# Performance work log

Hardware: AMD Instinct MI355X
Metric: run time of the kernel (lower is better)

## Reference

```python
import jax, jax.numpy as jnp
import numpy as np

EMBED_DIM = 1024
NUM_HEADS = 16
HEAD_DIM = EMBED_DIM // NUM_HEADS
SCALE = HEAD_DIM ** -0.5


def setup_inputs() -> dict:
    key = jax.random.key(0)
    ks = jax.random.split(key, 7)
    B, S, D = 4, 2048, EMBED_DIM
    return {
        "x": jax.random.normal(ks[0], (B, S, D), dtype=jnp.float32),
        "gamma": jnp.ones((D,), dtype=jnp.float32),
        "beta": jnp.zeros((D,), dtype=jnp.float32),
        "w_qkv": jax.random.normal(ks[1], (D, 3 * D), dtype=jnp.float32) * (D ** -0.5),
        "b_qkv": jax.random.normal(ks[2], (3 * D,), dtype=jnp.float32) * 0.02,
        "w_proj": jax.random.normal(ks[3], (D, D), dtype=jnp.float32) * (D ** -0.5),
        "b_proj": jax.random.normal(ks[4], (D,), dtype=jnp.float32) * 0.02,
    }


def reference(x, gamma, beta, w_qkv, b_qkv, w_proj, b_proj):
    B, S, D = x.shape
    # pre-norm LayerNorm (eps=1e-5, torch default)
    mu = jnp.mean(x, axis=-1, keepdims=True)
    var = jnp.mean(jnp.square(x - mu), axis=-1, keepdims=True)
    xn = (x - mu) * jax.lax.rsqrt(var + 1e-5) * gamma + beta
    # fused QKV projection -> (3, B, H, S, hd)
    qkv = (xn @ w_qkv + b_qkv).reshape(B, S, 3, NUM_HEADS, HEAD_DIM)
    qkv = jnp.transpose(qkv, (2, 0, 3, 1, 4))
    q, k, v = qkv[0], qkv[1], qkv[2]
    scores = jnp.einsum("bhqd,bhkd->bhqk", q, k) * SCALE
    attn = jax.nn.softmax(scores, axis=-1)  # dropout p=0 -> no-op
    ctx = jnp.einsum("bhqk,bhkd->bhqd", attn, v)
    ctx = jnp.transpose(ctx, (0, 2, 1, 3)).reshape(B, S, D)
    return ctx @ w_proj + b_proj
```

## Files before the change

### kernel.cpp

```cpp
#include <hip/hip_runtime.h>

typedef unsigned short ushort_t;
typedef __attribute__((ext_vector_type(8))) short bf16x8;
typedef __attribute__((ext_vector_type(4))) float f32x4;
typedef __attribute__((ext_vector_type(16))) float f32x16;
typedef __attribute__((ext_vector_type(2))) __bf16 bf16v2;

#define BN 4
#define SEQ 2048
#define DIM 1024
#define NH 16
#define HDIM 64
#define MROWS (BN*SEQ)
#define QSCALE 0.18033688011112042f

__device__ __forceinline__ float bf2f(ushort_t s){ return __uint_as_float(((unsigned)s) << 16); }
__device__ __forceinline__ ushort_t f2bf(float f){
  unsigned u = __float_as_uint(f);
  u += 0x7fffu + ((u >> 16) & 1u);
  return (ushort_t)(u >> 16);
}
__device__ __forceinline__ unsigned pack2(float a, float b){
  return (unsigned)f2bf(a) | ((unsigned)f2bf(b) << 16);
}

#define GLL16(gp, lp) __builtin_amdgcn_global_load_lds( \
    (const __attribute__((address_space(1))) void*)(gp), \
    (__attribute__((address_space(3))) void*)(lp), 16, 0, 0)

__global__ __launch_bounds__(256) void ln_kernel(const float* __restrict__ x,
                                                 const float* __restrict__ gamma,
                                                 const float* __restrict__ beta,
                                                 ushort_t* __restrict__ xnb)
{
  int row = blockIdx.x;
  int t = threadIdx.x;
  float4 v = ((const float4*)(x + (size_t)row * DIM))[t];
  float s = v.x+v.y+v.z+v.w;
  float ss = v.x*v.x+v.y*v.y+v.z*v.z+v.w*v.w;
  #pragma unroll
  for (int o = 32; o > 0; o >>= 1){ s += __shfl_down(s, o); ss += __shfl_down(ss, o); }
  __shared__ float red[10];
  int wid = t >> 6;
  if ((t & 63) == 0){ red[wid] = s; red[4+wid] = ss; }
  __syncthreads();
  if (t == 0){
    float S0 = red[0]+red[1]+red[2]+red[3];
    float SS = red[4]+red[5]+red[6]+red[7];
    float mu = S0 * (1.f/DIM);
    float var = SS * (1.f/DIM) - mu*mu;
    red[8] = mu; red[9] = rsqrtf(var + 1e-5f);
  }
  __syncthreads();
  float mu = red[8], rstd = red[9];
  float4 g = ((const float4*)gamma)[t];
  float4 b = ((const float4*)beta)[t];
  float f0 = (v.x - mu)*rstd*g.x + b.x;
  float f1 = (v.y - mu)*rstd*g.y + b.y;
  float f2 = (v.z - mu)*rstd*g.z + b.z;
  float f3 = (v.w - mu)*rstd*g.w + b.w;
  *(uint2*)(xnb + (size_t)row*DIM + t*4) = make_uint2(pack2(f0,f1), pack2(f2,f3));
}

__global__ __launch_bounds__(256) void cvt_t(const float* __restrict__ src,
                                             ushort_t* __restrict__ dst,
                                             int K, int N, float qscale)
{
  __shared__ float tile[64][65];
  int k0 = blockIdx.y*64, n0 = blockIdx.x*64;
  float sc = (n0 < 1024) ? qscale : 1.f;
  int t = threadIdx.x;
  int c = (t & 15) * 4, r = t >> 4;
  #pragma unroll
  for (int p = 0; p < 4; p++){
    float4 v = *(const float4*)(src + (size_t)(k0 + r + p*16)*N + n0 + c);
    tile[r+p*16][c]   = v.x; tile[r+p*16][c+1] = v.y;
    tile[r+p*16][c+2] = v.z; tile[r+p*16][c+3] = v.w;
  }
  __syncthreads();
  #pragma unroll
  for (int p = 0; p < 4; p++){
    int nn = r + p*16;
    ushort4 o;
    o.x = f2bf(tile[c+0][nn]*sc); o.y = f2bf(tile[c+1][nn]*sc);
    o.z = f2bf(tile[c+2][nn]*sc); o.w = f2bf(tile[c+3][nn]*sc);
    *(ushort4*)(dst + (size_t)(n0+nn)*K + k0 + c) = o;
  }
}

__global__ __launch_bounds__(256) void vtrans(const ushort_t* __restrict__ V,
                                              ushort_t* __restrict__ vt)
{
  __shared__ ushort_t tile[64][72];
  int bh = blockIdx.x >> 5, sc = blockIdx.x & 31;
  int t = threadIdx.x;
  const ushort_t* src = V + ((size_t)bh*SEQ + sc*64)*HDIM;
  #pragma unroll
  for (int p = 0; p < 2; p++){
    int idx = p*256 + t;
    int r = idx >> 3, c8 = (idx & 7)*8;
    *(uint4*)&tile[r][c8] = *(const uint4*)(src + (size_t)r*HDIM + c8);
  }
  __syncthreads();
  ushort_t* dstp = vt + ((size_t)(bh*32 + sc))*HDIM*64;
  #pragma unroll
  for (int p = 0; p < 2; p++){
    int idx = p*256 + t;
    int d = idx >> 3, c8 = (idx & 7)*8;
    uint4 u;
    u.x = (unsigned)tile[c8+0][d] | ((unsigned)tile[c8+1][d] << 16);
    u.y = (unsigned)tile[c8+2][d] | ((unsigned)tile[c8+3][d] << 16);
    u.z = (unsigned)tile[c8+4][d] | ((unsigned)tile[c8+5][d] << 16);
    u.w = (unsigned)tile[c8+6][d] | ((unsigned)tile[c8+7][d] << 16);
    *(uint4*)(dstp + (size_t)d*64 + c8) = u;
  }
}

template<int MODE, int NCOLS>
__global__ __launch_bounds__(256) void mfma_gemm(
    const ushort_t* __restrict__ A,
    const ushort_t* __restrict__ BT,
    const float* __restrict__ bias,
    void* __restrict__ Cv)
{
  __shared__ __align__(16) unsigned char smem[17408];
  ushort_t* AsL = (ushort_t*)smem;
  ushort_t* BsL = (ushort_t*)(smem + 8192);

  int t = threadIdx.x;
  int lane = t & 63, w = t >> 6;
  int col = lane & 15, quad = lane >> 4;
  int n0 = blockIdx.x * 128, m0 = blockIdx.y * 128;

  f32x4 acc[4][4];
  #pragma unroll
  for (int i = 0; i < 4; i++)
    #pragma unroll
    for (int j = 0; j < 4; j++) acc[i][j] = (f32x4){0.f,0.f,0.f,0.f};

  int mbase = (w & 1)*64 + col;
  int nbase = (w >> 1)*64 + col;

  int r0 = (2*w  )*16 + (lane >> 2);
  int r1 = (2*w+1)*16 + (lane >> 2);
  int c0 = (((lane & 3) ^ ((r0 & 3) ^ ((r0 >> 2) & 3))) << 3);
  int c1 = (((lane & 3) ^ ((r1 & 3) ^ ((r1 >> 2) & 3))) << 3);
  const ushort_t* gA0 = A  + (size_t)(m0 + r0)*DIM + c0;
  const ushort_t* gA1 = A  + (size_t)(m0 + r1)*DIM + c1;
  const ushort_t* gB0 = BT + (size_t)(n0 + r0)*DIM + c0;
  const ushort_t* gB1 = BT + (size_t)(n0 + r1)*DIM + c1;
  unsigned char* lA0 = smem        + (2*w  )*1024;
  unsigned char* lA1 = smem        + (2*w+1)*1024;
  unsigned char* lB0 = smem + 8192 + (2*w  )*1024;
  unsigned char* lB1 = smem + 8192 + (2*w+1)*1024;

  int ppos = ((quad ^ ((col & 3) ^ ((col >> 2) & 3))) << 3);

  for (int k0 = 0; k0 < DIM; k0 += 32){
    __syncthreads();
    GLL16(gA0 + k0, lA0);
    GLL16(gA1 + k0, lA1);
    GLL16(gB0 + k0, lB0);
    GLL16(gB1 + k0, lB1);
    __syncthreads();

    bf16x8 af[4], bfr[4];
    #pragma unroll
    for (int i = 0; i < 4; i++){
      af[i]  = *(const bf16x8*)&AsL[(mbase + i*16)*32 + ppos];
      bfr[i] = *(const bf16x8*)&BsL[(nbase + i*16)*32 + ppos];
    }
    #pragma unroll
    for (int mt = 0; mt < 4; mt++)
      #pragma unroll
      for (int nt = 0; nt < 4; nt++)
        acc[mt][nt] = __builtin_amdgcn_mfma_f32_16x16x32_bf16(af[mt], bfr[nt], acc[mt][nt], 0, 0, 0);
  }

  float bscale = (MODE == 2 && n0 < 1024) ? QSCALE : 1.f;
  float bv[4];
  #pragma unroll
  for (int nt = 0; nt < 4; nt++) bv[nt] = bias[n0 + (w>>1)*64 + nt*16 + col] * bscale;

  if (MODE == 2){
    ushort_t (*Cs)[136] = (ushort_t(*)[136])smem;
    ushort_t* C = (ushort_t*)Cv;
    #pragma unroll
    for (int ph = 0; ph < 2; ph++){
      __syncthreads();
      if ((w & 1) == ph){
        #pragma unroll
        for (int mt = 0; mt < 4; mt++)
          #pragma unroll
          for (int nt = 0; nt < 4; nt++)
            #pragma unroll
            for (int r = 0; r < 4; r++)
              Cs[mt*16 + quad*4 + r][(w>>1)*64 + nt*16 + col] = f2bf(acc[mt][nt][r] + bv[nt]);
      }
      __syncthreads();
      #pragma unroll
      for (int p = 0; p < 4; p++){
        int id = p*256 + t;
        int row = id >> 4, cc = id & 15;
        uint4 u = *(const uint4*)&Cs[row][cc*8];
        int m = m0 + ph*64 + row;
        int n = n0 + cc*8;
        int which = n >> 10, hh = (n >> 6) & 15, d = n & 63;
        int b_ = m >> 11, s_ = m & (SEQ-1);
        *(uint4*)&C[((((size_t)which*BN + b_)*NH + hh)*SEQ + s_)*HDIM + d] = u;
      }
    }
  } else {
    float (*Cf)[132] = (float(*)[132])smem;
    float* C = (float*)Cv;
    #pragma unroll
    for (int ph = 0; ph < 4; ph++){
      __syncthreads();
      if ((w & 1) == (ph >> 1)){
        #pragma unroll
        for (int mi = 0; mi < 2; mi++){
          int mt = (ph & 1)*2 + mi;
          #pragma unroll
          for (int nt = 0; nt < 4; nt++)
            #pragma unroll
            for (int r = 0; r < 4; r++)
              Cf[mi*16 + quad*4 + r][(w>>1)*64 + nt*16 + col] = acc[mt][nt][r] + bv[nt];
        }
      }
      __syncthreads();
      #pragma unroll
      for (int p = 0; p < 4; p++){
        int id = p*256 + t;
        int row = id >> 5, cc = id & 31;
        float4 v = *(const float4*)&Cf[row][cc*4];
        int m = m0 + ph*32 + row;
        *(float4*)(C + (size_t)m*NCOLS + n0 + cc*4) = v;
      }
    }
  }
}

__global__ __launch_bounds__(512) void attn_kernel(const ushort_t* __restrict__ qkv,
                                                   const ushort_t* __restrict__ vtp,
                                                   ushort_t* __restrict__ ctx)
{
  __shared__ __align__(16) unsigned char lds[53248];
  ushort_t* Ksm = (ushort_t*)lds;
  ushort_t* Vsm = (ushort_t*)(lds + 8192);

  int t = threadIdx.x;
  int lane = t & 63, w = t >> 6;
  int m32 = lane & 31, half = lane >> 5;
  int r7 = m32 & 7;
  int id = blockIdx.x;
  int bh = (id & 7) | ((id >> 6) << 3);
  int qb = (id >> 3) & 7;

  const size_t PL = (size_t)BN * NH * SEQ * HDIM;
  const ushort_t* Qg = qkv + (size_t)bh * (SEQ * HDIM);
  const ushort_t* Kg = Qg + PL;
  const ushort_t* Vt = vtp + (size_t)bh * 32 * (HDIM * 64);
  int qbase = qb*256 + w*32;

  bf16x8 qf[4];
  #pragma unroll
  for (int c = 0; c < 4; c++)
    qf[c] = *(const bf16x8*)(Qg + (size_t)(qbase + m32)*HDIM + c*16 + half*8);

  bf16x8 ones;
  #pragma unroll
  for (int i = 0; i < 8; i++) ones[i] = (short)0x3F80;

  f32x16 accO[2], accL;
  #pragma unroll
  for (int i = 0; i < 2; i++)
    #pragma unroll
    for (int r = 0; r < 16; r++) accO[i][r] = 0.f;
  #pragma unroll
  for (int r = 0; r < 16; r++) accL[r] = 0.f;

  int srow = t >> 3, och = t & 7;
  const ushort_t* kp0 = Kg + (size_t)srow*HDIM + och*8;
  const ushort_t* vp0 = Vt + (size_t)srow*64 + och*8;
  int wofs = srow*64 + ((och ^ (srow & 7)) << 3);

  uint4 kr = *(const uint4*)kp0;
  uint4 vr = *(const uint4*)vp0;

  for (int kt = 0; kt < 32; kt++){
    __syncthreads();
    *(uint4*)&Ksm[wofs] = kr;
    *(uint4*)&Vsm[wofs] = vr;
    __syncthreads();

    if (kt < 31){
      kr = *(const uint4*)(kp0 + (size_t)(kt+1)*64*HDIM);
      vr = *(const uint4*)(vp0 + (size_t)(kt+1)*HDIM*64);
    }

    bf16x8 pb[4];
    #pragma unroll
    for (int mt = 0; mt < 2; mt++){
      f32x16 z;
      #pragma unroll
      for (int r = 0; r < 16; r++) z[r] = 0.f;
      int rowb = (mt*32 + m32) * 64;
      #pragma unroll
      for (int c = 0; c < 4; c++){
        bf16x8 af = *(const bf16x8*)&Ksm[rowb + (((2*c + half) ^ r7) << 3)];
        z = __builtin_amdgcn_mfma_f32_32x32x16_bf16(af, qf[c], z, 0, 0, 0);
      }
      unsigned u[8];
      #pragma unroll
      for (int i = 0; i < 8; i++){
        float p0 = __builtin_amdgcn_exp2f(z[2*i]);
        float p1 = __builtin_amdgcn_exp2f(z[2*i+1]);
        bf16v2 hh; hh.x = (__bf16)p0; hh.y = (__bf16)p1;
        u[i] = __builtin_bit_cast(unsigned, hh);
      }
      #pragma unroll
      for (int cc = 0; cc < 2; cc++){
        union { uint4 q; bf16x8 b; } cvt;
        cvt.q = make_uint4(u[4*cc+0], u[4*cc+1], u[4*cc+2], u[4*cc+3]);
        pb[mt*2 + cc] = cvt.b;
      }
    }

    #pragma unroll
    for (int kc = 0; kc < 4; kc++){
      accL = __builtin_amdgcn_mfma_f32_32x32x16_bf16(ones, pb[kc], accL, 0, 0, 0);
      #pragma unroll
      for (int md = 0; md < 2; md++){
        int dd = md*32 + m32;
        int rowb = dd * 64;
        union { bf16x8 v8; uint2 u2[2]; } vv;
        vv.u2[0] = *(const uint2*)&Vsm[rowb + (((2*kc  ) ^ r7) << 3) + 4*half];
        vv.u2[1] = *(const uint2*)&Vsm[rowb + (((2*kc+1) ^ r7) << 3) + 4*half];
        accO[md] = __builtin_amdgcn_mfma_f32_32x32x16_bf16(vv.v8, pb[kc], accO[md], 0, 0, 0);
      }
    }
  }

  float inv = 1.f / accL[0];

  ushort_t (*Os)[72] = (ushort_t(*)[72])(lds + 16384 + w*4608);
  #pragma unroll
  for (int md = 0; md < 2; md++)
    #pragma unroll
    for (int g = 0; g < 4; g++){
      int d0 = 8*g + 4*half + 32*md;
      unsigned lo = pack2(accO[md][4*g+0]*inv, accO[md][4*g+1]*inv);
      unsigned hi = pack2(accO[md][4*g+2]*inv, accO[md][4*g+3]*inv);
      *(uint2*)&Os[m32][d0] = make_uint2(lo, hi);
    }

  int b_ = bh >> 4, h_ = bh & 15;
  #pragma unroll
  for (int k = 0; k < 4; k++){
    int row = k*8 + (lane >> 3);
    uint4 u = *(const uint4*)&Os[row][(lane & 7)*8];
    *(uint4*)(ctx + ((size_t)(b_*SEQ + qb*256 + w*32 + row))*DIM + h_*HDIM + (lane & 7)*8) = u;
  }
}

extern "C" void kernel_launch(void* const* d_in, const int* in_sizes, int n_in,
                              void* d_out, int out_size, void* d_ws, size_t ws_size,
                              hipStream_t stream)
{
  const float* x      = (const float*)d_in[0];
  const float* gamma  = (const float*)d_in[1];
  const float* beta   = (const float*)d_in[2];
  const float* w_qkv  = (const float*)d_in[3];
  const float* b_qkv  = (const float*)d_in[4];
  const float* w_proj = (const float*)d_in[5];
  const float* b_proj = (const float*)d_in[6];

  char* ws = (char*)d_ws;
  ushort_t* wqkvT  = (ushort_t*)ws;
  ushort_t* vt     = (ushort_t*)ws;
  ushort_t* wprojT = (ushort_t*)ws;
  ushort_t* qkv    = (ushort_t*)(ws + 16u*1024*1024);
  ushort_t* Vplane = (ushort_t*)(ws + 48u*1024*1024);
  ushort_t* ctx    = (ushort_t*)(ws + 48u*1024*1024);
  ushort_t* xnb    = (ushort_t*)d_out;

  ln_kernel<<<MROWS, 256, 0, stream>>>(x, gamma, beta, xnb);
  cvt_t<<<dim3(3*DIM/64, DIM/64), 256, 0, stream>>>(w_qkv, wqkvT, DIM, 3*DIM, QSCALE);
  mfma_gemm<2, 3*DIM><<<dim3(3*DIM/128, MROWS/128), 256, 0, stream>>>(
      xnb, wqkvT, b_qkv, qkv);
  vtrans<<<BN*NH*(SEQ/64), 256, 0, stream>>>(Vplane, vt);
  attn_kernel<<<BN*NH*(SEQ/256), 512, 0, stream>>>(qkv, vt, ctx);
  cvt_t<<<dim3(DIM/64, DIM/64), 256, 0, stream>>>(w_proj, wprojT, DIM, DIM, 1.f);
  mfma_gemm<0, DIM><<<dim3(DIM/128, MROWS/128), 256, 0, stream>>>(
      ctx, wprojT, b_proj, d_out);
}
```

Measured before the change: 305.1 us.

## Software-pipeline attention loop so QK^T of next tile overlaps PV of current

```diff
diff --git a/kernel.cpp b/kernel.cpp
--- a/kernel.cpp
+++ b/kernel.cpp
@@ -284,37 +284,36 @@
   const ushort_t* vp0 = Vt + (size_t)srow*64 + och*8;
   int wofs = srow*64 + ((och ^ (srow & 7)) << 3);
 
+  int rowb0 = (m32) * 64;
+  int rowb1 = (32 + m32) * 64;
+
   uint4 kr = *(const uint4*)kp0;
   uint4 vr = *(const uint4*)vp0;
-
-  for (int kt = 0; kt < 32; kt++){
-    __syncthreads();
-    *(uint4*)&Ksm[wofs] = kr;
+  *(uint4*)&Ksm[wofs] = kr;
+  kr = *(const uint4*)(kp0 + (size_t)64*HDIM);
+  __syncthreads();
+
+  bf16x8 pb[4];
+  {
+    f32x16 z0, z1;
+    #pragma unroll
+    for (int r = 0; r < 16; r++){ z0[r] = 0.f; z1[r] = 0.f; }
+    #pragma unroll
+    for (int c = 0; c < 4; c++){
+      bf16x8 a0 = *(const bf16x8*)&Ksm[rowb0 + (((2*c + half) ^ r7) << 3)];
+      bf16x8 a1 = *(const bf16x8*)&Ksm[rowb1 + (((2*c + half) ^ r7) << 3)];
+      z0 = __builtin_amdgcn_mfma_f32_32x32x16_bf16(a0, qf[c], z0, 0, 0, 0);
+      z1 = __builtin_amdgcn_mfma_f32_32x32x16_bf16(a1, qf[c], z1, 0, 0, 0);
+    }
     *(uint4*)&Vsm[wofs] = vr;
-    __syncthreads();
-
-    if (kt < 31){
-      kr = *(const uint4*)(kp0 + (size_t)(kt+1)*64*HDIM);
-      vr = *(const uint4*)(vp0 + (size_t)(kt+1)*HDIM*64);
-    }
-
-    bf16x8 pb[4];
+    vr = *(const uint4*)(vp0 + (size_t)HDIM*64);
     #pragma unroll
     for (int mt = 0; mt < 2; mt++){
-      f32x16 z;
-      #pragma unroll
-      for (int r = 0; r < 16; r++) z[r] = 0.f;
-      int rowb = (mt*32 + m32) * 64;
-      #pragma unroll
-      for (int c = 0; c < 4; c++){
-        bf16x8 af = *(const bf16x8*)&Ksm[rowb + (((2*c + half) ^ r7) << 3)];
-        z = __builtin_amdgcn_mfma_f32_32x32x16_bf16(af, qf[c], z, 0, 0, 0);
-      }
       unsigned u[8];
       #pragma unroll
       for (int i = 0; i < 8; i++){
-        float p0 = __builtin_amdgcn_exp2f(z[2*i]);
-        float p1 = __builtin_amdgcn_exp2f(z[2*i+1]);
+        float p0 = __builtin_amdgcn_exp2f(mt ? z1[2*i] : z0[2*i]);
+        float p1 = __builtin_amdgcn_exp2f(mt ? z1[2*i+1] : z0[2*i+1]);
         bf16v2 hh; hh.x = (__bf16)p0; hh.y = (__bf16)p1;
         u[i] = __builtin_bit_cast(unsigned, hh);
       }
@@ -325,19 +324,73 @@
         pb[mt*2 + cc] = cvt.b;
       }
     }
+  }
+  __syncthreads();
+
+  for (int i = 1; i <= 31; i++){
+    *(uint4*)&Ksm[wofs] = kr;
+    __syncthreads();
+
+    f32x16 z0, z1;
+    #pragma unroll
+    for (int r = 0; r < 16; r++){ z0[r] = 0.f; z1[r] = 0.f; }
+    #pragma unroll
+    for (int c = 0; c < 4; c++){
+      bf16x8 a0 = *(const bf16x8*)&Ksm[rowb0 + (((2*c + half) ^ r7) << 3)];
+      bf16x8 a1 = *(const bf16x8*)&Ksm[rowb1 + (((2*c + half) ^ r7) << 3)];
+      z0 = __builtin_amdgcn_mfma_f32_32x32x16_bf16(a0, qf[c], z0, 0, 0, 0);
+      z1 = __builtin_amdgcn_mfma_f32_32x32x16_bf16(a1, qf[c], z1, 0, 0, 0);
+    }
 
     #pragma unroll
     for (int kc = 0; kc < 4; kc++){
       accL = __builtin_amdgcn_mfma_f32_32x32x16_bf16(ones, pb[kc], accL, 0, 0, 0);
       #pragma unroll
       for (int md = 0; md < 2; md++){
-        int dd = md*32 + m32;
-        int rowb = dd * 64;
+        int rowb = (md*32 + m32) * 64;
         union { bf16x8 v8; uint2 u2[2]; } vv;
         vv.u2[0] = *(const uint2*)&Vsm[rowb + (((2*kc  ) ^ r7) << 3) + 4*half];
         vv.u2[1] = *(const uint2*)&Vsm[rowb + (((2*kc+1) ^ r7) << 3) + 4*half];
         accO[md] = __builtin_amdgcn_mfma_f32_32x32x16_bf16(vv.v8, pb[kc], accO[md], 0, 0, 0);
       }
+    }
+
+    #pragma unroll
+    for (int mt = 0; mt < 2; mt++){
+      unsigned u[8];
+      #pragma unroll
+      for (int i2 = 0; i2 < 8; i2++){
+        float p0 = __builtin_amdgcn_exp2f(mt ? z1[2*i2] : z0[2*i2]);
+        float p1 = __builtin_amdgcn_exp2f(mt ? z1[2*i2+1] : z0[2*i2+1]);
+        bf16v2 hh; hh.x = (__bf16)p0; hh.y = (__bf16)p1;
+        u[i2] = __builtin_bit_cast(unsigned, hh);
+      }
+      #pragma unroll
+      for (int cc = 0; cc < 2; cc++){
+        union { uint4 q; bf16x8 b; } cvt;
+        cvt.q = make_uint4(u[4*cc+0], u[4*cc+1], u[4*cc+2], u[4*cc+3]);
+        pb[mt*2 + cc] = cvt.b;
+      }
+    }
+
+    __syncthreads();
+    *(uint4*)&Vsm[wofs] = vr;
+    int nk = (i < 31) ? i + 1 : 31;
+    kr = *(const uint4*)(kp0 + (size_t)nk*64*HDIM);
+    vr = *(const uint4*)(vp0 + (size_t)nk*HDIM*64);
+  }
+
+  __syncthreads();
+  #pragma unroll
+  for (int kc = 0; kc < 4; kc++){
+    accL = __builtin_amdgcn_mfma_f32_32x32x16_bf16(ones, pb[kc], accL, 0, 0, 0);
+    #pragma unroll
+    for (int md = 0; md < 2; md++){
+      int rowb = (md*32 + m32) * 64;
+      union { bf16x8 v8; uint2 u2[2]; } vv;
+      vv.u2[0] = *(const uint2*)&Vsm[rowb + (((2*kc  ) ^ r7) << 3) + 4*half];
+      vv.u2[1] = *(const uint2*)&Vsm[rowb + (((2*kc+1) ^ r7) << 3) + 4*half];
+      accO[md] = __builtin_amdgcn_mfma_f32_32x32x16_bf16(vv.v8, pb[kc], accO[md], 0, 0, 0);
     }
   }
 
```

After: 313.9 us. +2.9%, slower.
